# Kernel optimization log

Measured on AMD Instinct MI355X. Metric: run time of the kernel, lower is better.

Reference implementation:

```python
import jax, jax.numpy as jnp
import numpy as np

B, S, E, H, D, F = 8, 512, 768, 12, 64, 3072
EPS = 1e-5
SQRT3 = np.float32(np.sqrt(3.0))


def _ln(x, g, b):
    m = jnp.mean(x, -1, keepdims=True)
    v = jnp.mean((x - m) ** 2, -1, keepdims=True)
    return (x - m) * jax.lax.rsqrt(v + EPS) * g + b


def _gelu_new(x):
    return 0.5 * x * (1.0 + jnp.tanh(0.7978845608028654 * (x + 0.044715 * x * x * x)))


def _heads(t):  # [B,T,E] -> [B,T,H,D]
    return t.reshape(t.shape[0], t.shape[1], H, D)


def _self_attn(xl, Wq, Wk, Wv, Wo, bo, mask):
    q = _heads(xl @ Wq)
    k = _heads(xl @ Wk)
    v = _heads(xl @ Wv)
    w = jnp.einsum('bqhd,bkhd->bhqk', q, k) / 8.0  # scale=True, sqrt(64)
    w = jnp.where(mask, -1e9, w)
    p = jax.nn.softmax(w, axis=-1)
    o = jnp.einsum('bhqk,bkhd->bqhd', p, v).reshape(xl.shape)
    present = jnp.stack([k.transpose(0, 2, 1, 3), v.transpose(0, 2, 1, 3)])  # [2,B,H,S,D]
    return o @ Wo + bo, present


def _cross_attn(xl, el, wq, bq, wk, bk, wv, bv, wp, bp, mask):
    q = _heads(xl @ wq + bq)
    k = _heads(el @ wk + bk)
    v = _heads(el @ wv + bv)
    w = jnp.einsum('bqhd,bkhd->bhqk', q, k) / 8.0
    w = jnp.where(mask, -1e4, w)
    p = jax.nn.softmax(w, axis=-1)
    o = jnp.einsum('bhqk,bkhd->bqhd', p, v).reshape(xl.shape)
    return o @ wp + bp  # Conv1D: x @ W + b


def _block(x, encoder_output, mask_queries, mask_sa, mask_enc, tau,
           Wq, Wk, Wv, Wo, bo,
           fcq_w, fcq_b, fck_w, fck_b, fcv_w, fcv_b, cproj_w, cproj_b,
           ln1_g, ln1_b, ln2_g, ln2_b,
           cfc_w, cfc_b, cproj2_w, cproj2_b,
           a1_w, a1_b, a2_w, a2_b, a3_w, a3_b):
    thr = jnp.asarray(tau, jnp.float32)
    sa, present = _self_attn(_ln(x, ln1_g, ln1_b), Wq, Wk, Wv, Wo, bo, mask_sa)
    a = x + sa  # resid dropout = identity (eval)
    al = _ln(a, ln1_g, ln1_b)

    def cross(idx):
        el = _ln(encoder_output[:, idx], ln1_g, ln1_b)
        return _cross_attn(al, el, fcq_w, fcq_b, fck_w, fck_b, fcv_w, fcv_b,
                           cproj_w, cproj_b, mask_enc)

    e1, e2, e3 = cross(0), cross(1), cross(2)

    def gate(e, w, b):
        alpha = jax.nn.sigmoid(jnp.concatenate([a, e], -1) @ w + b)
        lm = jnp.where(alpha > thr, 1.0, 0.0)
        vm = jnp.where(alpha < 1.0 - thr, 1.0, 0.0)
        return alpha * lm * a + (1.0 - alpha) * vm * e

    enc_att = (gate(e1, a1_w, a1_b) + gate(e2, a2_w, a2_b) + gate(e3, a3_w, a3_b)) / SQRT3
    aq = enc_att * mask_queries
    m = _gelu_new(_ln(aq, ln2_g, ln2_b) @ cfc_w + cfc_b) @ cproj2_w + cproj2_b
    out = (aq + m) * mask_queries
    return out, present


def setup_inputs() -> dict:
    key = jax.random.key(0)
    ks = jax.random.split(key, 40)
    p = lambda k, shp: (jax.random.normal(k, shp, jnp.float32) * 0.02)
    x = jax.random.normal(ks[0], (B, S, E), jnp.float32)
    encoder_output = jax.random.normal(ks[1], (B, 3, S, E), jnp.float32)
    mask_queries = jnp.ones((B, S, 1), jnp.float32)
    causal = ~jnp.tril(jnp.ones((S, S), bool))  # True = masked
    mask_self_attention = jnp.broadcast_to(causal[None, None], (B, 1, S, S))
    mask_encoder = jax.random.bernoulli(ks[2], 0.1, (B, 1, 1, S))
    d = dict(x=x, encoder_output=encoder_output, mask_queries=mask_queries,
             mask_self_attention=mask_self_attention, mask_encoder=mask_encoder,
             i=0, tau=0,
             Wq=p(ks[3], (E, E)), Wk=p(ks[4], (E, E)), Wv=p(ks[5], (E, E)),
             Wo=p(ks[6], (E, E)), bo=jnp.zeros((E,), jnp.float32),
             fcq_w=p(ks[7], (E, E)), fcq_b=jnp.zeros((E,), jnp.float32),
             fck_w=p(ks[8], (E, E)), fck_b=jnp.zeros((E,), jnp.float32),
             fcv_w=p(ks[9], (E, E)), fcv_b=jnp.zeros((E,), jnp.float32),
             cproj_w=p(ks[10], (E, E)), cproj_b=jnp.zeros((E,), jnp.float32),
             ln1_g=jnp.ones((E,), jnp.float32), ln1_b=jnp.zeros((E,), jnp.float32),
             ln2_g=jnp.ones((E,), jnp.float32), ln2_b=jnp.zeros((E,), jnp.float32),
             cfc_w=p(ks[11], (E, F)), cfc_b=jnp.zeros((F,), jnp.float32),
             cproj2_w=p(ks[12], (F, E)), cproj2_b=jnp.zeros((E,), jnp.float32),
             a1_w=p(ks[13], (2 * E, E)), a1_b=jnp.zeros((E,), jnp.float32),
             a2_w=p(ks[14], (2 * E, E)), a2_b=jnp.zeros((E,), jnp.float32),
             a3_w=p(ks[15], (2 * E, E)), a3_b=jnp.zeros((E,), jnp.float32))
    return d


def reference(x, encoder_output, mask_queries, mask_self_attention, mask_encoder, i, tau,
              Wq, Wk, Wv, Wo, bo,
              fcq_w, fcq_b, fck_w, fck_b, fcv_w, fcv_b, cproj_w, cproj_b,
              ln1_g, ln1_b, ln2_g, ln2_b,
              cfc_w, cfc_b, cproj2_w, cproj2_b,
              a1_w, a1_b, a2_w, a2_b, a3_w, a3_b):
    return _block(x, encoder_output, mask_queries, mask_self_attention, mask_encoder, tau,
                  Wq, Wk, Wv, Wo, bo,
                  fcq_w, fcq_b, fck_w, fck_b, fcv_w, fcv_b, cproj_w, cproj_b,
                  ln1_g, ln1_b, ln2_g, ln2_b,
                  cfc_w, cfc_b, cproj2_w, cproj2_b,
                  a1_w, a1_b, a2_w, a2_b, a3_w, a3_b)
```

## Files before the change

kernel.cpp:

```cpp
#include <hip/hip_runtime.h>
#include <hip/hip_bf16.h>
#include <math.h>

typedef __hip_bfloat16 bf16;
typedef __attribute__((ext_vector_type(8))) short s16x8;
typedef __attribute__((ext_vector_type(4))) float f32x4;

#define BB 8
#define SS 512
#define EE 768
#define HH 12
#define DD 64
#define FF 3072
#define NTOK (BB * SS)
#define NE ((size_t)NTOK * EE)

#define TM 128
#define TN 128
#define TK 64

#define QT 64
#define KT 64

#define FLAG_RES  4
#define FLAG_GELU 8
#define FLAG_FIN  16
#define FLAG_CBSD 32
#define FLAG_QKV  128
#define FLAG_KV   256
#define FLAG_GSEG 512

#define AS1 const __attribute__((address_space(1))) void*
#define AS3 __attribute__((address_space(3))) void*

__device__ __forceinline__ float gelu_new(float x) {
    float u2 = 1.5957691216057308f * (x + 0.044715f * x * x * x);
    return x / (1.0f + __expf(-u2));
}

__global__ __launch_bounds__(256) void tcast_all_kernel(
    const float* s0, const float* s1, const float* s2, const float* s3,
    const float* s4, const float* s5, const float* s6, const float* s7,
    const float* s8, const float* s9, const float* s10, const float* s11,
    const float* s12,
    bf16* d0, bf16* d1, bf16* d2, bf16* d3, bf16* d4, bf16* d5, bf16* d6,
    bf16* d7, bf16* d8, bf16* d9, bf16* d10, bf16* d11, bf16* d12)
{
    const int start[14] = {0, 576, 1152, 1728, 2304, 2880, 3456, 4032,
                           4608, 5760, 6912, 8064, 10368, 12672};
    const float* srcs[13] = {s0,s1,s2,s3,s4,s5,s6,s7,s8,s9,s10,s11,s12};
    bf16* dsts[13] = {d0,d1,d2,d3,d4,d5,d6,d7,d8,d9,d10,d11,d12};

    int bid = blockIdx.x;
    int idx = 0;
    #pragma unroll
    for (int i = 1; i < 13; ++i) if (bid >= start[i]) idx = i;
    int R = (idx < 8) ? 768 : (idx < 11) ? 1536 : (idx == 11) ? 768 : 3072;
    int C = (idx < 8) ? 768 : (idx < 11) ? 768 : (idx == 11) ? 3072 : 768;
    const float* src = srcs[idx];
    bf16* dst = dsts[idx];

    int t = bid - start[idx];
    int gx = C >> 5;
    int c0 = (t % gx) << 5;
    int r0 = (t / gx) << 5;

    __shared__ float tb[32][33];
    int tid = threadIdx.x;
    int x = tid & 31, y = tid >> 5;
    #pragma unroll
    for (int i = 0; i < 4; ++i) {
        int r = y + i * 8;
        tb[r][x] = src[(size_t)(r0 + r) * C + c0 + x];
    }
    __syncthreads();
    #pragma unroll
    for (int i = 0; i < 4; ++i) {
        int c = y + i * 8;
        dst[(size_t)(c0 + c) * R + r0 + x] = __float2bfloat16(tb[x][c]);
    }
}

__global__ __launch_bounds__(256) void biascopy_kernel(
    const float* fckb, const float* fcvb, const float* a0, const float* a1,
    const float* a2, float* kvb, float* gb)
{
    int i = blockIdx.x * 256 + threadIdx.x;
    int seg = i / 768, off = i % 768;
    if (seg == 0)      kvb[off]        = fckb[off];
    else if (seg == 1) kvb[768 + off]  = fcvb[off];
    else if (seg == 2) gb[off]         = a0[off];
    else if (seg == 3) gb[768 + off]   = a1[off];
    else               gb[1536 + off]  = a2[off];
}

__global__ __launch_bounds__(256) void ln_kernel(
    const float* __restrict__ in, bf16* __restrict__ out,
    const float* __restrict__ g, const float* __restrict__ bta, int encmode)
{
    int row = blockIdx.x;
    const float* x;
    if (encmode) {
        int idx = row >> 12, b = (row >> 9) & 7, s = row & 511;
        x = in + (((size_t)b * 3 + idx) * SS + s) * EE;
    } else {
        x = in + (size_t)row * EE;
    }
    int tid = threadIdx.x;

    float v0 = x[tid], v1 = x[tid + 256], v2 = x[tid + 512];
    float s1 = v0 + v1 + v2;
    float s2 = v0 * v0 + v1 * v1 + v2 * v2;
    #pragma unroll
    for (int o = 32; o > 0; o >>= 1) {
        s1 += __shfl_down(s1, o);
        s2 += __shfl_down(s2, o);
    }
    __shared__ float r1[4], r2[4];
    if ((tid & 63) == 0) { r1[tid >> 6] = s1; r2[tid >> 6] = s2; }
    __syncthreads();
    float mean = (r1[0] + r1[1] + r1[2] + r1[3]) * (1.0f / 768.0f);
    float ssq  = (r2[0] + r2[1] + r2[2] + r2[3]) * (1.0f / 768.0f);
    float rstd = rsqrtf(ssq - mean * mean + 1e-5f);

    bf16* y = out + (size_t)row * EE;
    y[tid]       = __float2bfloat16((v0 - mean) * rstd * g[tid]       + bta[tid]);
    y[tid + 256] = __float2bfloat16((v1 - mean) * rstd * g[tid + 256] + bta[tid + 256]);
    y[tid + 512] = __float2bfloat16((v2 - mean) * rstd * g[tid + 512] + bta[tid + 512]);
}

template <int FLAGS>
__global__ __launch_bounds__(256) void mgemm_kernel(
    const bf16* __restrict__ A, const bf16* __restrict__ A2,
    const bf16* __restrict__ Wt, const float* __restrict__ bias,
    float* __restrict__ Cf, bf16* __restrict__ Cb, bf16* __restrict__ Cb2,
    int ldcb, const float* __restrict__ Rsrc, const float* __restrict__ maskq,
    int Nn, int K, int lda)
{
    constexpr bool f_res  = FLAGS & FLAG_RES;
    constexpr bool f_gelu = FLAGS & FLAG_GELU;
    constexpr bool f_fin  = FLAGS & FLAG_FIN;
    constexpr bool f_cbsd = FLAGS & FLAG_CBSD;
    constexpr bool f_qkv  = FLAGS & FLAG_QKV;
    constexpr bool f_kv   = FLAGS & FLAG_KV;
    constexpr bool f_gseg = FLAGS & FLAG_GSEG;

    __shared__ __align__(16) bf16 smem[2 * (TM * TK + TN * TK)];
    const int BUFE = TM * TK + TN * TK;
    int tid = threadIdx.x;
    int w = tid >> 6, l = tid & 63;
    int row0 = blockIdx.x * TM, col0 = blockIdx.y * TN;

    int wr = (w >> 1) * 64, wc = (w & 1) * 64;
    int lr = l & 15, lg = l >> 4;

    const bf16* Wb = Wt;
    const float* bb_ = bias;
    if constexpr (f_gseg) {
        int seg = row0 >> 12;
        Wb = Wt + (size_t)seg * 1536 * 768;
        bb_ = bias + seg * 768;
    }

    f32x4 acc[4][4];
    #pragma unroll
    for (int m = 0; m < 4; ++m)
        #pragma unroll
        for (int n = 0; n < 4; ++n) acc[m][n] = (f32x4){0.f, 0.f, 0.f, 0.f};

    auto stage = [&](int buf, int kb) {
        bf16* As_ = smem + buf * BUFE;
        bf16* Bs_ = As_ + TM * TK;
        #pragma unroll
        for (int i = 0; i < 4; ++i) {
            int e = (i * 256 + tid) * 8;
            int r = e >> 6;
            int c = (e & 63) ^ ((r & 7) << 3);
            const bf16* asrc;
            if constexpr (f_gseg) {
                int kg = kb + c;
                if (kg < 768) asrc = A  + (size_t)((row0 + r) & 4095) * lda + kg;
                else          asrc = A2 + (size_t)(row0 + r) * lda + (kg - 768);
            } else {
                asrc = A + (size_t)(row0 + r) * lda + kb + c;
            }
            __builtin_amdgcn_global_load_lds((AS1)asrc,
                (AS3)((char*)As_ + i * 4096 + w * 1024), 16, 0, 0);
            __builtin_amdgcn_global_load_lds((AS1)(Wb + (size_t)(col0 + r) * K + kb + c),
                (AS3)((char*)Bs_ + i * 4096 + w * 1024), 16, 0, 0);
        }
    };

    int nk = K / TK;
    stage(0, 0);
    for (int t = 0; t < nk; ++t) {
        int cur = t & 1;
        if (t + 1 < nk) {
            stage(cur ^ 1, (t + 1) * TK);
            asm volatile("s_waitcnt vmcnt(8)" ::: "memory");
        } else {
            asm volatile("s_waitcnt vmcnt(0)" ::: "memory");
        }
        __builtin_amdgcn_s_barrier();
        __builtin_amdgcn_sched_barrier(0);

        const char* As = (const char*)(smem + cur * BUFE);
        const char* Bs = As + TM * TK * 2;
        __builtin_amdgcn_s_setprio(1);
        #pragma unroll
        for (int ks = 0; ks < 2; ++ks) {
            s16x8 af[4], bfr[4];
            #pragma unroll
            for (int m = 0; m < 4; ++m) {
                int row = wr + m * 16 + lr;
                af[m] = *(const s16x8*)(As + row * 128 +
                          ((ks * 64 + lg * 16) ^ ((row & 7) << 4)));
            }
            #pragma unroll
            for (int n = 0; n < 4; ++n) {
                int row = wc + n * 16 + lr;
                bfr[n] = *(const s16x8*)(Bs + row * 128 +
                          ((ks * 64 + lg * 16) ^ ((row & 7) << 4)));
            }
            #pragma unroll
            for (int m = 0; m < 4; ++m)
                #pragma unroll
                for (int n = 0; n < 4; ++n)
                    acc[m][n] = __builtin_amdgcn_mfma_f32_16x16x32_bf16(
                        af[m], bfr[n], acc[m][n], 0, 0, 0);
        }
        __builtin_amdgcn_s_setprio(0);
        asm volatile("s_waitcnt lgkmcnt(0)" ::: "memory");
        __builtin_amdgcn_s_barrier();
        __builtin_amdgcn_sched_barrier(0);
    }

    int gh0 = (col0 + wc) >> 6;
    bool vquad = (f_qkv && gh0 >= 24) || (f_kv && gh0 >= 12);
    bf16* T = smem + w * 4096;

    #pragma unroll
    for (int m = 0; m < 4; ++m) {
        #pragma unroll
        for (int n = 0; n < 4; ++n) {
            #pragma unroll
            for (int j = 0; j < 4; ++j) {
                int row = row0 + wr + m * 16 + lg * 4 + j;
                int col = col0 + wc + n * 16 + lr;
                size_t lin = (size_t)row * Nn + col;
                float v = acc[m][n][j];
                if (bb_)                 v += bb_[col];
                if constexpr (f_res)     v += Rsrc[lin];
                if constexpr (f_gelu)    v = gelu_new(v);
                if constexpr (f_fin)     v = (Rsrc[lin] + v) * maskq[row];
                int bb = row >> 9, s = row & 511;
                int gh = col >> 6, d = col & 63;
                if constexpr (f_qkv) {
                    if (gh < 12) {
                        Cb[(((size_t)bb * HH + gh) * SS + s) * DD + d] = __float2bfloat16(v);
                    } else if (gh < 24) {
                        Cf[(((size_t)bb * HH + (gh - 12)) * SS + s) * DD + d] = v;
                        Cb[NE + (((size_t)bb * HH + (gh - 12)) * SS + s) * DD + d] = __float2bfloat16(v);
                    } else {
                        Cf[NE + (((size_t)bb * HH + (gh - 24)) * SS + s) * DD + d] = v;
                        int rl = m * 16 + lg * 4 + j, cl = n * 16 + lr;
                        *(bf16*)((char*)T + cl * 128 + ((rl * 2) ^ ((cl & 7) << 4))) =
                            __float2bfloat16(v);
                    }
                } else if constexpr (f_kv) {
                    if (gh < 12) {
                        Cb[(((size_t)bb * HH + gh) * SS + s) * DD + d] = __float2bfloat16(v);
                    } else {
                        int rl = m * 16 + lg * 4 + j, cl = n * 16 + lr;
                        *(bf16*)((char*)T + cl * 128 + ((rl * 2) ^ ((cl & 7) << 4))) =
                            __float2bfloat16(v);
                    }
                } else if constexpr (f_cbsd) {
                    Cb[(((size_t)bb * HH + gh) * SS + s) * DD + d] = __float2bfloat16(v);
                } else {
                    if (Cf) Cf[lin] = v;
                    if (Cb) Cb[(size_t)row * ldcb + col] = __float2bfloat16(v);
                }
            }
        }
    }

    if constexpr (f_qkv || f_kv) {
        if (vquad) {
            int b2 = (row0 + wr) >> 9;
            int s0 = (row0 + wr) & 511;
            int hV = gh0 - (f_qkv ? 24 : 12);
            bf16* vb = Cb2 + (((size_t)b2 * HH + hV) * DD) * SS + s0;
            #pragma unroll
            for (int p = 0; p < 8; ++p) {
                int dl = p * 8 + (l >> 3);
                int ch = l & 7;
                int cs = ch ^ (dl & 7);
                s16x8 vv = *(const s16x8*)((char*)T + dl * 128 + cs * 16);
                *(s16x8*)(vb + (size_t)dl * SS + ch * 8) = vv;
            }
        }
    }
}

__global__ __launch_bounds__(256) void fattn2_kernel(
    const bf16* __restrict__ Qb, const bf16* __restrict__ Kb,
    const bf16* __restrict__ Vb, const int* __restrict__ maskE,
    bf16* __restrict__ Out, int causal)
{
    int bh = blockIdx.x, qt = blockIdx.y;
    int bp = bh / HH, h = bh % HH;
    int bq = bp & 7;
    int tid = threadIdx.x;
    int w = tid >> 6, l = tid & 63;
    int lr = l & 15, g = l >> 4;

    __shared__ __align__(16) bf16 Qs[64 * 64];
    __shared__ __align__(16) bf16 Ks[64 * 64];
    __shared__ __align__(16) bf16 Vs[64 * 64];
    __shared__ __align__(16) bf16 Ps[64 * 64];

    int p0 = w * 1024 + l * 16;
    {
        const char* qg = (const char*)(Qb + (((size_t)bq * HH + h) * SS + qt * QT) * DD);
        #pragma unroll
        for (int i = 0; i < 2; ++i) {
            int p = i * 4096 + p0;
            int row = p >> 7, cb = p & 127;
            int scb = cb ^ ((row & 7) << 4);
            __builtin_amdgcn_global_load_lds((AS1)(qg + row * 128 + scb),
                (AS3)((char*)Qs + i * 4096 + w * 1024), 16, 0, 0);
        }
    }

    float mrun[4], lrun[4];
    f32x4 oacc[4];
    #pragma unroll
    for (int j = 0; j < 4; ++j) { mrun[j] = -3.0e38f; lrun[j] = 0.f; }
    #pragma unroll
    for (int n = 0; n < 4; ++n) oacc[n] = (f32x4){0.f, 0.f, 0.f, 0.f};

    int ntiles = causal ? (qt + 1) : (SS / KT);
    int qrow_base = w * 16;

    for (int kt = 0; kt < ntiles; ++kt) {
        const char* kg = (const char*)(Kb + ((size_t)bh * SS + kt * KT) * DD);
        const char* vg = (const char*)(Vb + (size_t)bh * DD * SS + (size_t)kt * KT);
        #pragma unroll
        for (int i = 0; i < 2; ++i) {
            int p = i * 4096 + p0;
            int row = p >> 7, cb = p & 127;
            int scb = cb ^ ((row & 7) << 4);
            __builtin_amdgcn_global_load_lds((AS1)(kg + row * 128 + scb),
                (AS3)((char*)Ks + i * 4096 + w * 1024), 16, 0, 0);
            __builtin_amdgcn_global_load_lds((AS1)(vg + (size_t)row * (SS * 2) + scb),
                (AS3)((char*)Vs + i * 4096 + w * 1024), 16, 0, 0);
        }
        int km[4];
        if (maskE) {
            #pragma unroll
            for (int n = 0; n < 4; ++n)
                km[n] = maskE[(size_t)bq * SS + kt * KT + n * 16 + lr];
        }
        __syncthreads();

        f32x4 sacc[4];
        #pragma unroll
        for (int n = 0; n < 4; ++n) sacc[n] = (f32x4){0.f, 0.f, 0.f, 0.f};
        #pragma unroll
        for (int ks = 0; ks < 2; ++ks) {
            int qrow = qrow_base + lr;
            s16x8 aq = *(const s16x8*)((const char*)Qs +
                        qrow * 128 + ((ks * 64 + g * 16) ^ ((qrow & 7) << 4)));
            #pragma unroll
            for (int n = 0; n < 4; ++n) {
                int krow = n * 16 + lr;
                s16x8 bk = *(const s16x8*)((const char*)Ks +
                            krow * 128 + ((ks * 64 + g * 16) ^ ((krow & 7) << 4)));
                sacc[n] = __builtin_amdgcn_mfma_f32_16x16x32_bf16(aq, bk, sacc[n], 0, 0, 0);
            }
        }

        #pragma unroll
        for (int n = 0; n < 4; ++n) {
            #pragma unroll
            for (int j = 0; j < 4; ++j) {
                float v = sacc[n][j] * 0.125f;
                if (causal) {
                    if (kt == qt && (n * 16 + lr > qrow_base + 4 * g + j)) v = -3.0e38f;
                } else {
                    if (km[n] != 0) v = -1e4f;
                }
                sacc[n][j] = v;
            }
        }

        float mx[4];
        #pragma unroll
        for (int j = 0; j < 4; ++j)
            mx[j] = fmaxf(fmaxf(sacc[0][j], sacc[1][j]), fmaxf(sacc[2][j], sacc[3][j]));
        #pragma unroll
        for (int msk = 1; msk < 16; msk <<= 1) {
            #pragma unroll
            for (int j = 0; j < 4; ++j) mx[j] = fmaxf(mx[j], __shfl_xor(mx[j], msk));
        }
        float rs[4], psum[4];
        #pragma unroll
        for (int j = 0; j < 4; ++j) {
            float mn = fmaxf(mrun[j], mx[j]);
            rs[j] = __expf(mrun[j] - mn);
            mrun[j] = mn;
            psum[j] = 0.f;
        }
        #pragma unroll
        for (int n = 0; n < 4; ++n) {
            #pragma unroll
            for (int j = 0; j < 4; ++j) {
                float p = __expf(sacc[n][j] - mrun[j]);
                psum[j] += p;
                int prow = qrow_base + 4 * g + j;
                int key = n * 16 + lr;
                *(bf16*)((char*)Ps + prow * 128 + ((2 * key) ^ ((prow & 7) << 4))) =
                    __float2bfloat16(p);
            }
        }
        #pragma unroll
        for (int msk = 1; msk < 16; msk <<= 1) {
            #pragma unroll
            for (int j = 0; j < 4; ++j) psum[j] += __shfl_xor(psum[j], msk);
        }
        #pragma unroll
        for (int j = 0; j < 4; ++j) lrun[j] = lrun[j] * rs[j] + psum[j];
        #pragma unroll
        for (int n = 0; n < 4; ++n) {
            #pragma unroll
            for (int j = 0; j < 4; ++j) oacc[n][j] *= rs[j];
        }

        #pragma unroll
        for (int ks = 0; ks < 2; ++ks) {
            int prow = qrow_base + lr;
            s16x8 ap = *(const s16x8*)((const char*)Ps +
                        prow * 128 + ((ks * 64 + g * 16) ^ ((prow & 7) << 4)));
            #pragma unroll
            for (int n = 0; n < 4; ++n) {
                int vrow = n * 16 + lr;
                s16x8 bv = *(const s16x8*)((const char*)Vs +
                            vrow * 128 + ((ks * 64 + g * 16) ^ ((vrow & 7) << 4)));
                oacc[n] = __builtin_amdgcn_mfma_f32_16x16x32_bf16(ap, bv, oacc[n], 0, 0, 0);
            }
        }
        __syncthreads();
    }

    float inv[4];
    #pragma unroll
    for (int j = 0; j < 4; ++j) inv[j] = 1.0f / lrun[j];
    #pragma unroll
    for (int n = 0; n < 4; ++n) {
        #pragma unroll
        for (int j = 0; j < 4; ++j) {
            int q = qt * QT + qrow_base + 4 * g + j;
            int d = n * 16 + lr;
            Out[((size_t)bp * SS + q) * EE + h * DD + d] =
                __float2bfloat16(oacc[n][j] * inv[j]);
        }
    }
}

__global__ __launch_bounds__(256) void gate3ln_kernel(
    const float* __restrict__ logits, const float* __restrict__ a,
    const bf16* __restrict__ e, float* __restrict__ acc, bf16* __restrict__ lnout,
    const int* __restrict__ tau, const float* __restrict__ maskq,
    const float* __restrict__ g, const float* __restrict__ bta)
{
    int row = blockIdx.x;
    int tid = threadIdx.x;
    float thr = (float)tau[0];
    float mq = maskq[row] * 0.57735026918962576f;
    size_t base = (size_t)row * EE;

    float aq[3];
    float s1 = 0.f, s2 = 0.f;
    #pragma unroll
    for (int c = 0; c < 3; ++c) {
        size_t i = base + tid + c * 256;
        float av = a[i];
        float r = 0.f;
        #pragma unroll
        for (int idx = 0; idx < 3; ++idx) {
            float lg = logits[(size_t)idx * NE + i];
            float ev = __bfloat162float(e[(size_t)idx * NE + i]);
            float al = 1.0f / (1.0f + __expf(-lg));
            float lm = (al > thr) ? 1.0f : 0.0f;
            float vm = (al < 1.0f - thr) ? 1.0f : 0.0f;
            r += al * lm * av + (1.0f - al) * vm * ev;
        }
        float v = r * mq;
        acc[i] = v;
        aq[c] = v;
        s1 += v;
        s2 += v * v;
    }
    #pragma unroll
    for (int o = 32; o > 0; o >>= 1) {
        s1 += __shfl_down(s1, o);
        s2 += __shfl_down(s2, o);
    }
    __shared__ float r1[4], r2[4];
    if ((tid & 63) == 0) { r1[tid >> 6] = s1; r2[tid >> 6] = s2; }
    __syncthreads();
    float mean = (r1[0] + r1[1] + r1[2] + r1[3]) * (1.0f / 768.0f);
    float ssq  = (r2[0] + r2[1] + r2[2] + r2[3]) * (1.0f / 768.0f);
    float rstd = rsqrtf(ssq - mean * mean + 1e-5f);

    bf16* y = lnout + base;
    #pragma unroll
    for (int c = 0; c < 3; ++c) {
        int col = tid + c * 256;
        y[col] = __float2bfloat16((aq[c] - mean) * rstd * g[col] + bta[col]);
    }
}

extern "C" void kernel_launch(void* const* d_in, const int* in_sizes, int n_in,
                              void* d_out, int out_size, void* d_ws, size_t ws_size,
                              hipStream_t stream)
{
    const float* x        = (const float*)d_in[0];
    const float* enc      = (const float*)d_in[1];
    const float* maskq    = (const float*)d_in[2];
    const int*   mask_enc = (const int*)d_in[4];
    const int*   tau      = (const int*)d_in[6];
    const float* Wq = (const float*)d_in[7];
    const float* Wk = (const float*)d_in[8];
    const float* Wv = (const float*)d_in[9];
    const float* Wo = (const float*)d_in[10];
    const float* bo = (const float*)d_in[11];
    const float* fcq_w = (const float*)d_in[12];
    const float* fcq_b = (const float*)d_in[13];
    const float* fck_w = (const float*)d_in[14];
    const float* fck_b = (const float*)d_in[15];
    const float* fcv_w = (const float*)d_in[16];
    const float* fcv_b = (const float*)d_in[17];
    const float* cproj_w = (const float*)d_in[18];
    const float* cproj_b = (const float*)d_in[19];
    const float* ln1_g = (const float*)d_in[20];
    const float* ln1_b = (const float*)d_in[21];
    const float* ln2_g = (const float*)d_in[22];
    const float* ln2_b = (const float*)d_in[23];
    const float* cfc_w = (const float*)d_in[24];
    const float* cfc_b = (const float*)d_in[25];
    const float* cproj2_w = (const float*)d_in[26];
    const float* cproj2_b = (const float*)d_in[27];
    const float* aw[3] = {(const float*)d_in[28], (const float*)d_in[30], (const float*)d_in[32]};
    const float* ab[3] = {(const float*)d_in[29], (const float*)d_in[31], (const float*)d_in[33]};

    float* out   = (float*)d_out;
    float* kpres = out + NE;

    float* ws  = (float*)d_ws;
    float* a     = ws;
    float* acc   = ws + NE;
    float* R     = ws + 2 * NE;
    bf16*  kb_c   = (bf16*)R;
    bf16*  vb_c   = kb_c + 3 * NE;
    float* logits = R;
    bf16*  mlphb  = (bf16*)R;

    bf16* bbase = (bf16*)(ws + 5 * NE);
    bf16* lnb   = bbase;
    bf16* atts  = bbase;
    bf16* lnenc = bbase + NE;
    bf16* attc  = lnenc;
    bf16* a_bf  = bbase + 4 * NE;
    bf16* e_bf  = bbase + 5 * NE;
    bf16* qbhb  = bbase + 8 * NE;
    bf16* kbhb  = bbase + 9 * NE;
    bf16* vbhb  = bbase + 10 * NE;
    bf16* wp    = bbase + 11 * NE;
    bf16* WqkvT = wp;          wp += 3 * 768 * 768;
    bf16* WoT = wp;            wp += 768 * 768;
    bf16* fcqT = wp;           wp += 768 * 768;
    bf16* fckvT = wp;          wp += 2 * 768 * 768;
    bf16* cprojT = wp;         wp += 768 * 768;
    bf16* awT = wp;            wp += (size_t)3 * 1536 * 768;
    bf16* cfcT = wp;           wp += (size_t)768 * 3072;
    bf16* cproj2T = wp;        wp += (size_t)3072 * 768;
    float* kvb = (float*)wp;
    float* gb  = kvb + 1536;

    dim3 blk(256);

    tcast_all_kernel<<<12672, blk, 0, stream>>>(
        Wq, Wk, Wv, Wo, fcq_w, fck_w, fcv_w, cproj_w,
        aw[0], aw[1], aw[2], cfc_w, cproj2_w,
        WqkvT, WqkvT + 768 * 768, WqkvT + 2 * 768 * 768, WoT, fcqT,
        fckvT, fckvT + 768 * 768, cprojT,
        awT, awT + 1536 * 768, awT + 2 * 1536 * 768, cfcT, cproj2T);
    biascopy_kernel<<<15, blk, 0, stream>>>(fck_b, fcv_b, ab[0], ab[1], ab[2], kvb, gb);

    ln_kernel<<<NTOK, blk, 0, stream>>>(x, lnb, ln1_g, ln1_b, 0);
    mgemm_kernel<FLAG_QKV><<<dim3(32, 18), blk, 0, stream>>>(lnb, nullptr, WqkvT, nullptr,
        kpres, qbhb, vbhb, 0, nullptr, nullptr, 2304, 768, 768);
    fattn2_kernel<<<dim3(96, 8), blk, 0, stream>>>(qbhb, kbhb, vbhb, nullptr, atts, 1);
    mgemm_kernel<FLAG_RES><<<dim3(32, 6), blk, 0, stream>>>(atts, nullptr, WoT, bo,
        a, a_bf, nullptr, 768, x, nullptr, 768, 768, 768);
    ln_kernel<<<NTOK, blk, 0, stream>>>(a, lnb, ln1_g, ln1_b, 0);
    mgemm_kernel<FLAG_CBSD><<<dim3(32, 6), blk, 0, stream>>>(lnb, nullptr, fcqT, fcq_b,
        nullptr, qbhb, nullptr, 0, nullptr, nullptr, 768, 768, 768);
    ln_kernel<<<3 * NTOK, blk, 0, stream>>>(enc, lnenc, ln1_g, ln1_b, 1);
    mgemm_kernel<FLAG_KV><<<dim3(96, 12), blk, 0, stream>>>(lnenc, nullptr, fckvT, kvb,
        nullptr, kb_c, vb_c, 0, nullptr, nullptr, 1536, 768, 768);
    fattn2_kernel<<<dim3(288, 8), blk, 0, stream>>>(qbhb, kb_c, vb_c, mask_enc, attc, 0);
    mgemm_kernel<0><<<dim3(96, 6), blk, 0, stream>>>(attc, nullptr, cprojT, cproj_b,
        nullptr, e_bf, nullptr, 768, nullptr, nullptr, 768, 768, 768);
    mgemm_kernel<FLAG_GSEG><<<dim3(96, 6), blk, 0, stream>>>(a_bf, e_bf, awT, gb,
        logits, nullptr, nullptr, 0, nullptr, nullptr, 768, 1536, 768);
    gate3ln_kernel<<<NTOK, blk, 0, stream>>>(logits, a, e_bf, acc, lnb,
        tau, maskq, ln2_g, ln2_b);
    mgemm_kernel<FLAG_GELU><<<dim3(32, 24), blk, 0, stream>>>(lnb, nullptr, cfcT, cfc_b,
        nullptr, mlphb, nullptr, 3072, nullptr, nullptr, 3072, 768, 768);
    mgemm_kernel<FLAG_FIN><<<dim3(32, 6), blk, 0, stream>>>(mlphb, nullptr, cproj2T, cproj2_b,
        out, nullptr, nullptr, 0, acc, maskq, 768, 3072, 3072);
}
```

Before: 632.2 us.

## Merge launches: fold bias copy, batch layernorms, fuse QKV and cross KV GEMMs

Folds the bias copy into the weight transpose-cast kernel as extra blocks. Merges the input and encoder layernorms into one launch, and fuses the self-attention QKV GEMM with the cross-attention KV GEMM into a single grid that dispatches by block index. The aim is to cut launch count and tail underutilisation by giving the GPU larger combined grids. The fused GEMM kernel may take on register pressure from both template instantiations, and the cross KV work now sits on the critical path before self-attention.

```diff
diff --git a/kernel.cpp b/kernel.cpp
--- a/kernel.cpp
+++ b/kernel.cpp
@@ -44,14 +44,27 @@
     const float* s8, const float* s9, const float* s10, const float* s11,
     const float* s12,
     bf16* d0, bf16* d1, bf16* d2, bf16* d3, bf16* d4, bf16* d5, bf16* d6,
-    bf16* d7, bf16* d8, bf16* d9, bf16* d10, bf16* d11, bf16* d12)
-{
+    bf16* d7, bf16* d8, bf16* d9, bf16* d10, bf16* d11, bf16* d12,
+    const float* fckb, const float* fcvb, const float* a0, const float* a1,
+    const float* a2, float* kvb, float* gb)
+{
+    int bid = blockIdx.x;
+    int tid = threadIdx.x;
+    if (bid >= 12672) {
+        int i = (bid - 12672) * 256 + tid;
+        int seg = i / 768, off = i % 768;
+        if (seg == 0)      kvb[off]       = fckb[off];
+        else if (seg == 1) kvb[768 + off] = fcvb[off];
+        else if (seg == 2) gb[off]        = a0[off];
+        else if (seg == 3) gb[768 + off]  = a1[off];
+        else               gb[1536 + off] = a2[off];
+        return;
+    }
     const int start[14] = {0, 576, 1152, 1728, 2304, 2880, 3456, 4032,
                            4608, 5760, 6912, 8064, 10368, 12672};
     const float* srcs[13] = {s0,s1,s2,s3,s4,s5,s6,s7,s8,s9,s10,s11,s12};
     bf16* dsts[13] = {d0,d1,d2,d3,d4,d5,d6,d7,d8,d9,d10,d11,d12};
 
-    int bid = blockIdx.x;
     int idx = 0;
     #pragma unroll
     for (int i = 1; i < 13; ++i) if (bid >= start[i]) idx = i;
@@ -66,7 +79,6 @@
     int r0 = (t / gx) << 5;
 
     __shared__ float tb[32][33];
-    int tid = threadIdx.x;
     int x = tid & 31, y = tid >> 5;
     #pragma unroll
     for (int i = 0; i < 4; ++i) {
@@ -81,33 +93,10 @@
     }
 }
 
-__global__ __launch_bounds__(256) void biascopy_kernel(
-    const float* fckb, const float* fcvb, const float* a0, const float* a1,
-    const float* a2, float* kvb, float* gb)
-{
-    int i = blockIdx.x * 256 + threadIdx.x;
-    int seg = i / 768, off = i % 768;
-    if (seg == 0)      kvb[off]        = fckb[off];
-    else if (seg == 1) kvb[768 + off]  = fcvb[off];
-    else if (seg == 2) gb[off]         = a0[off];
-    else if (seg == 3) gb[768 + off]   = a1[off];
-    else               gb[1536 + off]  = a2[off];
-}
-
-__global__ __launch_bounds__(256) void ln_kernel(
-    const float* __restrict__ in, bf16* __restrict__ out,
-    const float* __restrict__ g, const float* __restrict__ bta, int encmode)
-{
-    int row = blockIdx.x;
-    const float* x;
-    if (encmode) {
-        int idx = row >> 12, b = (row >> 9) & 7, s = row & 511;
-        x = in + (((size_t)b * 3 + idx) * SS + s) * EE;
-    } else {
-        x = in + (size_t)row * EE;
-    }
-    int tid = threadIdx.x;
-
+__device__ __forceinline__ void ln_body(
+    const float* __restrict__ x, bf16* __restrict__ y,
+    const float* __restrict__ g, const float* __restrict__ bta, int tid)
+{
     float v0 = x[tid], v1 = x[tid + 256], v2 = x[tid + 512];
     float s1 = v0 + v1 + v2;
     float s2 = v0 * v0 + v1 * v1 + v2 * v2;
@@ -122,15 +111,38 @@
     float mean = (r1[0] + r1[1] + r1[2] + r1[3]) * (1.0f / 768.0f);
     float ssq  = (r2[0] + r2[1] + r2[2] + r2[3]) * (1.0f / 768.0f);
     float rstd = rsqrtf(ssq - mean * mean + 1e-5f);
-
-    bf16* y = out + (size_t)row * EE;
     y[tid]       = __float2bfloat16((v0 - mean) * rstd * g[tid]       + bta[tid]);
     y[tid + 256] = __float2bfloat16((v1 - mean) * rstd * g[tid + 256] + bta[tid + 256]);
     y[tid + 512] = __float2bfloat16((v2 - mean) * rstd * g[tid + 512] + bta[tid + 512]);
 }
 
+__global__ __launch_bounds__(256) void ln_kernel(
+    const float* __restrict__ in, bf16* __restrict__ out,
+    const float* __restrict__ g, const float* __restrict__ bta)
+{
+    int row = blockIdx.x;
+    ln_body(in + (size_t)row * EE, out + (size_t)row * EE, g, bta, threadIdx.x);
+}
+
+__global__ __launch_bounds__(256) void ln_all_kernel(
+    const float* __restrict__ x, const float* __restrict__ enc,
+    bf16* __restrict__ outx, bf16* __restrict__ outenc,
+    const float* __restrict__ g, const float* __restrict__ bta)
+{
+    int row = blockIdx.x;
+    if (row < NTOK) {
+        ln_body(x + (size_t)row * EE, outx + (size_t)row * EE, g, bta, threadIdx.x);
+    } else {
+        int r = row - NTOK;
+        int idx = r >> 12, b = (r >> 9) & 7, s = r & 511;
+        ln_body(enc + (((size_t)b * 3 + idx) * SS + s) * EE,
+                outenc + (size_t)r * EE, g, bta, threadIdx.x);
+    }
+}
+
 template <int FLAGS>
-__global__ __launch_bounds__(256) void mgemm_kernel(
+__device__ __forceinline__ void mgemm_body(
+    int bx, int by, bf16* smem,
     const bf16* __restrict__ A, const bf16* __restrict__ A2,
     const bf16* __restrict__ Wt, const float* __restrict__ bias,
     float* __restrict__ Cf, bf16* __restrict__ Cb, bf16* __restrict__ Cb2,
@@ -145,11 +157,10 @@
     constexpr bool f_kv   = FLAGS & FLAG_KV;
     constexpr bool f_gseg = FLAGS & FLAG_GSEG;
 
-    __shared__ __align__(16) bf16 smem[2 * (TM * TK + TN * TK)];
     const int BUFE = TM * TK + TN * TK;
     int tid = threadIdx.x;
     int w = tid >> 6, l = tid & 63;
-    int row0 = blockIdx.x * TM, col0 = blockIdx.y * TN;
+    int row0 = bx * TM, col0 = by * TN;
 
     int wr = (w >> 1) * 64, wc = (w & 1) * 64;
     int lr = l & 15, lg = l >> 4;
@@ -303,6 +314,38 @@
     }
 }
 
+template <int FLAGS>
+__global__ __launch_bounds__(256) void mgemm_kernel(
+    const bf16* __restrict__ A, const bf16* __restrict__ A2,
+    const bf16* __restrict__ Wt, const float* __restrict__ bias,
+    float* __restrict__ Cf, bf16* __restrict__ Cb, bf16* __restrict__ Cb2,
+    int ldcb, const float* __restrict__ Rsrc, const float* __restrict__ maskq,
+    int Nn, int K, int lda)
+{
+    __shared__ __align__(16) bf16 smem[2 * (TM * TK + TN * TK)];
+    mgemm_body<FLAGS>(blockIdx.x, blockIdx.y, smem, A, A2, Wt, bias,
+                      Cf, Cb, Cb2, ldcb, Rsrc, maskq, Nn, K, lda);
+}
+
+__global__ __launch_bounds__(256) void qkvkv_kernel(
+    const bf16* __restrict__ lnb, const bf16* __restrict__ lnenc,
+    const bf16* __restrict__ WqkvT, const bf16* __restrict__ fckvT,
+    const float* __restrict__ kvb,
+    float* __restrict__ kpres, bf16* __restrict__ qbhb, bf16* __restrict__ vbhb,
+    bf16* __restrict__ kb_c, bf16* __restrict__ vb_c)
+{
+    __shared__ __align__(16) bf16 smem[2 * (TM * TK + TN * TK)];
+    int bid = blockIdx.x;
+    if (bid < 576) {
+        mgemm_body<FLAG_QKV>(bid & 31, bid >> 5, smem, lnb, nullptr, WqkvT, nullptr,
+                             kpres, qbhb, vbhb, 0, nullptr, nullptr, 2304, 768, 768);
+    } else {
+        int t = bid - 576;
+        mgemm_body<FLAG_KV>(t % 96, t / 96, smem, lnenc, nullptr, fckvT, kvb,
+                            nullptr, kb_c, vb_c, 0, nullptr, nullptr, 1536, 768, 768);
+    }
+}
+
 __global__ __launch_bounds__(256) void fattn2_kernel(
     const bf16* __restrict__ Qb, const bf16* __restrict__ Kb,
     const bf16* __restrict__ Vb, const int* __restrict__ maskE,
@@ -591,26 +634,22 @@
 
     dim3 blk(256);
 
-    tcast_all_kernel<<<12672, blk, 0, stream>>>(
+    tcast_all_kernel<<<12687, blk, 0, stream>>>(
         Wq, Wk, Wv, Wo, fcq_w, fck_w, fcv_w, cproj_w,
         aw[0], aw[1], aw[2], cfc_w, cproj2_w,
         WqkvT, WqkvT + 768 * 768, WqkvT + 2 * 768 * 768, WoT, fcqT,
         fckvT, fckvT + 768 * 768, cprojT,
-        awT, awT + 1536 * 768, awT + 2 * 1536 * 768, cfcT, cproj2T);
-    biascopy_kernel<<<15, blk, 0, stream>>>(fck_b, fcv_b, ab[0], ab[1], ab[2], kvb, gb);
-
-    ln_kernel<<<NTOK, blk, 0, stream>>>(x, lnb, ln1_g, ln1_b, 0);
-    mgemm_kernel<FLAG_QKV><<<dim3(32, 18), blk, 0, stream>>>(lnb, nullptr, WqkvT, nullptr,
-        kpres, qbhb, vbhb, 0, nullptr, nullptr, 2304, 768, 768);
+        awT, awT + 1536 * 768, awT + 2 * 1536 * 768, cfcT, cproj2T,
+        fck_b, fcv_b, ab[0], ab[1], ab[2], kvb, gb);
+    ln_all_kernel<<<4 * NTOK, blk, 0, stream>>>(x, enc, lnb, lnenc, ln1_g, ln1_b);
+    qkvkv_kernel<<<1728, blk, 0, stream>>>(lnb, lnenc, WqkvT, fckvT, kvb,
+        kpres, qbhb, vbhb, kb_c, vb_c);
     fattn2_kernel<<<dim3(96, 8), blk, 0, stream>>>(qbhb, kbhb, vbhb, nullptr, atts, 1);
     mgemm_kernel<FLAG_RES><<<dim3(32, 6), blk, 0, stream>>>(atts, nullptr, WoT, bo,
         a, a_bf, nullptr, 768, x, nullptr, 768, 768, 768);
-    ln_kernel<<<NTOK, blk, 0, stream>>>(a, lnb, ln1_g, ln1_b, 0);
+    ln_kernel<<<NTOK, blk, 0, stream>>>(a, lnb, ln1_g, ln1_b);
     mgemm_kernel<FLAG_CBSD><<<dim3(32, 6), blk, 0, stream>>>(lnb, nullptr, fcqT, fcq_b,
         nullptr, qbhb, nullptr, 0, nullptr, nullptr, 768, 768, 768);
-    ln_kernel<<<3 * NTOK, blk, 0, stream>>>(enc, lnenc, ln1_g, ln1_b, 1);
-    mgemm_kernel<FLAG_KV><<<dim3(96, 12), blk, 0, stream>>>(lnenc, nullptr, fckvT, kvb,
-        nullptr, kb_c, vb_c, 0, nullptr, nullptr, 1536, 768, 768);
     fattn2_kernel<<<dim3(288, 8), blk, 0, stream>>>(qbhb, kb_c, vb_c, mask_enc, attc, 0);
     mgemm_kernel<0><<<dim3(96, 6), blk, 0, stream>>>(attc, nullptr, cprojT, cproj_b,
         nullptr, e_bf, nullptr, 768, nullptr, nullptr, 768, 768, 768);
```

Result: faster. 574.7 us (-9.1%).
